# Performance work log

Hardware: AMD Instinct MI355X
Metric: run time of the kernel (lower is better)

## Reference

```python
import jax, jax.numpy as jnp
import numpy as np

N_NODES = 40000
N_EDGES = 640000
BATCH = 2
IN_DIM = 3
HID = 128
OUT_DIM = 3


def setup_inputs() -> dict:
    key = jax.random.key(0)
    ks = jax.random.split(key, 16)
    p = jax.random.normal(ks[0], (BATCH, N_NODES, IN_DIM), dtype=jnp.float32)
    edge_rows = jax.random.randint(ks[1], (N_EDGES,), 0, N_NODES, dtype=jnp.int32)
    edge_cols = jax.random.randint(ks[2], (N_EDGES,), 0, N_NODES, dtype=jnp.int32)
    # normalize_sparse_matrix: divide each nonzero (value 1.0) by the row's nonzero count
    deg = jax.ops.segment_sum(jnp.ones((N_EDGES,), jnp.float32), edge_rows, num_segments=N_NODES)
    adj_vals = 1.0 / deg[edge_rows]  # every used row has deg >= 1
    s = 0.05
    # initial Linear(3 -> 128)
    W_init = jax.random.normal(ks[3], (IN_DIM, HID), jnp.float32) * s
    b_init = jnp.zeros((HID,), jnp.float32)
    # 4 GraphConvs inside the two blocks (all 128->128), each has filter + self_filter
    Wf_blocks = jax.random.normal(ks[4], (4, HID, HID), jnp.float32) * s
    bf_blocks = jnp.zeros((4, HID), jnp.float32)
    Ws_blocks = jax.random.normal(ks[5], (4, HID, HID), jnp.float32) * s
    bs_blocks = jnp.zeros((4, HID), jnp.float32)
    # final GraphConvLayer (128 -> 3)
    Wf_out = jax.random.normal(ks[6], (HID, OUT_DIM), jnp.float32) * s
    bf_out = jnp.zeros((OUT_DIM,), jnp.float32)
    Ws_out = jax.random.normal(ks[7], (HID, OUT_DIM), jnp.float32) * s
    bs_out = jnp.zeros((OUT_DIM,), jnp.float32)
    return dict(p=p, adj_vals=adj_vals, edge_rows=edge_rows, edge_cols=edge_cols,
                W_init=W_init, b_init=b_init,
                Wf_blocks=Wf_blocks, bf_blocks=bf_blocks,
                Ws_blocks=Ws_blocks, bs_blocks=bs_blocks,
                Wf_out=Wf_out, bf_out=bf_out, Ws_out=Ws_out, bs_out=bs_out)


def reference(p, adj_vals, edge_rows, edge_cols,
              W_init, b_init,
              Wf_blocks, bf_blocks, Ws_blocks, bs_blocks,
              Wf_out, bf_out, Ws_out, bs_out):
    n = p.shape[1]

    def spmm(xb):  # xb: [N, d] -> A @ xb via edge-list scatter-add
        return jax.ops.segment_sum(adj_vals[:, None] * xb[edge_cols], edge_rows, num_segments=n)

    spmm_b = jax.vmap(spmm)  # [B, N, d]

    def gconv(x, Wf, bf, Ws, bs):
        # sparse path: self_filter(x) + filter(spmm(adj, x))
        return (x @ Ws + bs) + (spmm_b(x) @ Wf + bf)

    x = p @ W_init + b_init  # [B, N, HID]
    for blk in range(2):  # two GraphConvBlocks, residual, no shortcut (dims equal)
        net = gconv(jax.nn.relu(x), Wf_blocks[2 * blk], bf_blocks[2 * blk],
                    Ws_blocks[2 * blk], bs_blocks[2 * blk])
        dx = gconv(jax.nn.relu(net), Wf_blocks[2 * blk + 1], bf_blocks[2 * blk + 1],
                   Ws_blocks[2 * blk + 1], bs_blocks[2 * blk + 1])
        x = x + dx
    # final GraphConvLayer 128 -> 3
    out = gconv(jax.nn.relu(x), Wf_out, bf_out, Ws_out, bs_out)
    return out
```

## Files before the change

kernel.cpp:

```cpp
#include <hip/hip_runtime.h>


typedef unsigned short u16;
typedef unsigned int   u32;
typedef __bf16 bf8_t __attribute__((ext_vector_type(8)));
typedef float  f4_t  __attribute__((ext_vector_type(4)));

#define N_NODES 40000
#define N_EDGES 640000
#define BN      80000

__device__ __forceinline__ float bf2f(u16 u) {
  union { u32 i; float f; } v; v.i = ((u32)u) << 16; return v.f;
}
__device__ __forceinline__ u16 f2bf(float f) {
  union { float f; u32 i; } v; v.f = f;
  u32 i = v.i;
  return (u16)((i + 0x7FFFu + ((i >> 16) & 1u)) >> 16);
}
__device__ __forceinline__ float asf(u32 i) {
  union { u32 u; float f; } v; v.u = i; return v.f;
}
__device__ __forceinline__ u32 pack2(float a, float b) {
  return (u32)f2bf(a) | ((u32)f2bf(b) << 16);
}
__device__ __forceinline__ float lo2f(u32 v) { return asf(v << 16); }
__device__ __forceinline__ float hi2f(u32 v) { return asf(v & 0xffff0000u); }
__device__ __forceinline__ u32 relu2(u32 v) {
  u32 r = v;
  if (r & 0x8000u)     r &= 0xffff0000u;
  if (r & 0x80000000u) r &= 0x0000ffffu;
  return r;
}

__global__ void fill_kernel(float* __restrict__ out, int n, float v) {
  int i = blockIdx.x * 256 + threadIdx.x;
  if (i < n) out[i] = v;
}

__global__ void hist_kernel(const int* __restrict__ rows, int* __restrict__ cnt) {
  int e = blockIdx.x * 256 + threadIdx.x;
  if (e < N_EDGES) atomicAdd(&cnt[rows[e]], 1);
}

__global__ void scan1_kernel(const int* __restrict__ cnt, int* __restrict__ row_ptr,
                             int* __restrict__ blocksum) {
  __shared__ int sm[256];
  int t = threadIdx.x;
  int row = blockIdx.x * 256 + t;
  int v = (row < N_NODES) ? cnt[row] : 0;
  sm[t] = v; __syncthreads();
  for (int off = 1; off < 256; off <<= 1) {
    int u = (t >= off) ? sm[t - off] : 0;
    __syncthreads();
    sm[t] += u;
    __syncthreads();
  }
  if (row < N_NODES) row_ptr[row] = sm[t] - v;
  if (t == 255) blocksum[blockIdx.x] = sm[255];
}

__global__ void scan2_kernel(int* __restrict__ blocksum, int* __restrict__ row_ptr, int nblk) {
  __shared__ int sm[256];
  int t = threadIdx.x;
  int v = (t < nblk) ? blocksum[t] : 0;
  sm[t] = v; __syncthreads();
  for (int off = 1; off < 256; off <<= 1) {
    int u = (t >= off) ? sm[t - off] : 0;
    __syncthreads();
    sm[t] += u;
    __syncthreads();
  }
  if (t < nblk) blocksum[t] = sm[t] - v;
  if (t == 255) row_ptr[N_NODES] = sm[255];
}

__global__ void scan3_kernel(int* __restrict__ row_ptr, const int* __restrict__ blocksum,
                             int* __restrict__ cnt) {
  int row = blockIdx.x * 256 + threadIdx.x;
  if (row < N_NODES) {
    int rp = row_ptr[row] + blocksum[blockIdx.x];
    row_ptr[row] = rp;
    cnt[row] = rp;
  }
}

__global__ void scatter_kernel(const int* __restrict__ rows, const int* __restrict__ cols,
                               int* __restrict__ cur, int* __restrict__ cols_s) {
  int e = blockIdx.x * 256 + threadIdx.x;
  if (e < N_EDGES) {
    int r = rows[e];
    int pos = atomicAdd(&cur[r], 1);
    cols_s[pos] = cols[e];
  }
}

__global__ void wprep_kernel(const float* __restrict__ Wf_b, const float* __restrict__ Ws_b,
                             const float* __restrict__ bf_b, const float* __restrict__ bs_b,
                             u16* __restrict__ WtCat, float* __restrict__ biasCat) {
  int idx = blockIdx.x * 256 + threadIdx.x;
  int g = idx >> 15, rem = idx & 32767;
  int h = rem >> 8, k = rem & 255;
  float v = (k < 128) ? Ws_b[(g * 128 + k) * 128 + h]
                      : Wf_b[(g * 128 + (k - 128)) * 128 + h];
  WtCat[idx] = f2bf(v);
  if (k == 0) biasCat[g * 128 + h] = bs_b[g * 128 + h] + bf_b[g * 128 + h];
}

__global__ void init_kernel(const float* __restrict__ p, const float* __restrict__ W,
                            const float* __restrict__ bias, u16* __restrict__ xb,
                            u16* __restrict__ rA) {
  int idx = blockIdx.x * 256 + threadIdx.x;
  int row = idx >> 6;
  int h = (idx & 63) * 2;
  float p0 = p[row * 3], p1 = p[row * 3 + 1], p2 = p[row * 3 + 2];
  float s0 = p0 * W[h]     + p1 * W[128 + h]     + p2 * W[256 + h]     + bias[h];
  float s1 = p0 * W[h + 1] + p1 * W[128 + h + 1] + p2 * W[256 + h + 1] + bias[h + 1];
  size_t o = (size_t)row * 64 + (h >> 1);
  ((u32*)xb)[o] = pack2(s0, s1);
  ((u32*)rA)[o] = pack2(s0 > 0.f ? s0 : 0.f, s1 > 0.f ? s1 : 0.f);
}

#define ACC8(u)                                                           \
  a0 += asf((u).x << 16); a1 += asf((u).x & 0xffff0000u);                 \
  a2 += asf((u).y << 16); a3 += asf((u).y & 0xffff0000u);                 \
  a4 += asf((u).z << 16); a5 += asf((u).z & 0xffff0000u);                 \
  a6 += asf((u).w << 16); a7 += asf((u).w & 0xffff0000u);

__global__ void spmm_kernel(const int* __restrict__ row_ptr, const int* __restrict__ cols_s,
                            const u16* __restrict__ xin, u16* __restrict__ yout) {
  int b = blockIdx.x & 1;
  int row = (blockIdx.x >> 1) * 4 + (threadIdx.x >> 6);
  int l = threadIdx.x & 63;
  int g = l >> 4, sl = l & 15;
  int s = row_ptr[row], e = row_ptr[row + 1];
  const uint4* X = (const uint4*)xin + (size_t)b * 640000 + sl;
  float a0 = 0.f, a1 = 0.f, a2 = 0.f, a3 = 0.f, a4 = 0.f, a5 = 0.f, a6 = 0.f, a7 = 0.f;
  int i = s;
  for (; i + 7 < e; i += 8) {
    int c0 = cols_s[i + g], c1 = cols_s[i + 4 + g];
    uint4 u0 = X[(size_t)c0 * 16];
    uint4 u1 = X[(size_t)c1 * 16];
    ACC8(u0); ACC8(u1);
  }
  for (; i + 3 < e; i += 4) {
    int c = cols_s[i + g];
    uint4 u = X[(size_t)c * 16];
    ACC8(u);
  }
  if (i + g < e) {
    int c = cols_s[i + g];
    uint4 u = X[(size_t)c * 16];
    ACC8(u);
  }
  a0 += __shfl_xor(a0, 16); a1 += __shfl_xor(a1, 16); a2 += __shfl_xor(a2, 16); a3 += __shfl_xor(a3, 16);
  a4 += __shfl_xor(a4, 16); a5 += __shfl_xor(a5, 16); a6 += __shfl_xor(a6, 16); a7 += __shfl_xor(a7, 16);
  a0 += __shfl_xor(a0, 32); a1 += __shfl_xor(a1, 32); a2 += __shfl_xor(a2, 32); a3 += __shfl_xor(a3, 32);
  a4 += __shfl_xor(a4, 32); a5 += __shfl_xor(a5, 32); a6 += __shfl_xor(a6, 32); a7 += __shfl_xor(a7, 32);
  if (g == 0) {
    float sc = (e > s) ? 1.f / (float)(e - s) : 0.f;
    uint4 o;
    o.x = pack2(a0 * sc, a1 * sc);
    o.y = pack2(a2 * sc, a3 * sc);
    o.z = pack2(a4 * sc, a5 * sc);
    o.w = pack2(a6 * sc, a7 * sc);
    *((uint4*)yout + (size_t)b * 640000 + (size_t)row * 16 + sl) = o;
  }
}

#define TS 136
template <int MODE>
__global__ __launch_bounds__(256, 4) void gemm_kernel(
    const u16* __restrict__ rin, const u16* __restrict__ yin,
    const u16* __restrict__ WtCat, const float* __restrict__ biasCat, int g,
    u16* __restrict__ rout, u16* __restrict__ xresid) {
  __shared__ __align__(16) u16 lds[18432];
  u16* ldsA = lds;
  u16* ldsW = lds + 9216;
  int tid = threadIdx.x;
  int m0 = blockIdx.x * 128;
  int li = tid & 15, q = (tid >> 4) & 3, wv = tid >> 6;
  int wmo = (wv >> 1) * 64, wno = (wv & 1) * 64;

  f4_t acc[4][4];
#pragma unroll
  for (int i = 0; i < 4; ++i)
#pragma unroll
    for (int j = 0; j < 4; ++j) acc[i][j] = (f4_t){0.f, 0.f, 0.f, 0.f};

  const u16* Wsrc = WtCat + (size_t)g * 32768;

  for (int kb = 0; kb < 256; kb += 64) {
    __syncthreads();
    const u16* srcA = (kb < 128) ? (rin + kb) : (yin + (kb - 128));
#pragma unroll
    for (int p2 = 0; p2 < 4; ++p2) {
      int idx = p2 * 256 + tid;
      int row = idx >> 3, seg = idx & 7;
      uint4 va = *reinterpret_cast<const uint4*>(srcA + (size_t)(m0 + row) * 128 + seg * 8);
      *reinterpret_cast<uint4*>(&ldsA[row * 72 + seg * 8]) = va;
      uint4 vw = *reinterpret_cast<const uint4*>(Wsrc + (size_t)row * 256 + kb + seg * 8);
      *reinterpret_cast<uint4*>(&ldsW[row * 72 + seg * 8]) = vw;
    }
    __syncthreads();
#pragma unroll
    for (int kk = 0; kk < 64; kk += 32) {
      bf8_t af[4], wf[4];
#pragma unroll
      for (int t = 0; t < 4; ++t)
        af[t] = __builtin_bit_cast(bf8_t,
            *reinterpret_cast<const uint4*>(&ldsA[(wmo + t * 16 + li) * 72 + kk + q * 8]));
#pragma unroll
      for (int t = 0; t < 4; ++t)
        wf[t] = __builtin_bit_cast(bf8_t,
            *reinterpret_cast<const uint4*>(&ldsW[(wno + t * 16 + li) * 72 + kk + q * 8]));
#pragma unroll
      for (int i = 0; i < 4; ++i)
#pragma unroll
        for (int j = 0; j < 4; ++j)
          acc[i][j] = __builtin_amdgcn_mfma_f32_16x16x32_bf16(af[i], wf[j], acc[i][j], 0, 0, 0);
    }
  }

  float bias[4];
#pragma unroll
  for (int j = 0; j < 4; ++j) bias[j] = biasCat[g * 128 + wno + j * 16 + li];

  __syncthreads();
#pragma unroll
  for (int i = 0; i < 4; ++i)
#pragma unroll
    for (int j = 0; j < 4; ++j)
#pragma unroll
      for (int r2 = 0; r2 < 4; ++r2) {
        int m = wmo + i * 16 + q * 4 + r2;
        int col = wno + j * 16 + li;
        lds[m * TS + col] = f2bf(acc[i][j][r2] + bias[j]);
      }
  __syncthreads();

#pragma unroll
  for (int p2 = 0; p2 < 8; ++p2) {
    int idx = p2 * 256 + tid;
    int row = idx >> 4, ch = idx & 15;
    uint4 cv = *reinterpret_cast<const uint4*>(&lds[row * TS + ch * 8]);
    size_t gid = (size_t)(m0 + row) * 16 + ch;
    if (MODE == 0) {
      uint4 o;
      o.x = relu2(cv.x); o.y = relu2(cv.y); o.z = relu2(cv.z); o.w = relu2(cv.w);
      ((uint4*)rout)[gid] = o;
    } else {
      uint4 xv = ((const uint4*)xresid)[gid];
      uint4 nx, nr;
      float x0, x1;
      x0 = lo2f(xv.x) + lo2f(cv.x); x1 = hi2f(xv.x) + hi2f(cv.x);
      nx.x = pack2(x0, x1); nr.x = pack2(x0 > 0.f ? x0 : 0.f, x1 > 0.f ? x1 : 0.f);
      x0 = lo2f(xv.y) + lo2f(cv.y); x1 = hi2f(xv.y) + hi2f(cv.y);
      nx.y = pack2(x0, x1); nr.y = pack2(x0 > 0.f ? x0 : 0.f, x1 > 0.f ? x1 : 0.f);
      x0 = lo2f(xv.z) + lo2f(cv.z); x1 = hi2f(xv.z) + hi2f(cv.z);
      nx.z = pack2(x0, x1); nr.z = pack2(x0 > 0.f ? x0 : 0.f, x1 > 0.f ? x1 : 0.f);
      x0 = lo2f(xv.w) + lo2f(cv.w); x1 = hi2f(xv.w) + hi2f(cv.w);
      nx.w = pack2(x0, x1); nr.w = pack2(x0 > 0.f ? x0 : 0.f, x1 > 0.f ? x1 : 0.f);
      ((uint4*)xresid)[gid] = nx;
      ((uint4*)rout)[gid] = nr;
    }
  }
}

__global__ void zproj_kernel(const u16* __restrict__ rA,
                             const float* __restrict__ Wfo, const float* __restrict__ Wso,
                             const float* __restrict__ bfo, const float* __restrict__ bso,
                             float4* __restrict__ zf4, float4* __restrict__ zs4) {
  int row = blockIdx.x * 4 + (threadIdx.x >> 6);
  int l = threadIdx.x & 63;
  u32 ra = ((const u32*)rA)[(size_t)row * 64 + l];
  float r0 = asf(ra << 16), r1 = asf(ra & 0xffff0000u);
  int ch = l * 2;
  float f0 = r0 * Wfo[ch * 3 + 0] + r1 * Wfo[ch * 3 + 3];
  float f1 = r0 * Wfo[ch * 3 + 1] + r1 * Wfo[ch * 3 + 4];
  float f2 = r0 * Wfo[ch * 3 + 2] + r1 * Wfo[ch * 3 + 5];
  float s0 = r0 * Wso[ch * 3 + 0] + r1 * Wso[ch * 3 + 3];
  float s1 = r0 * Wso[ch * 3 + 1] + r1 * Wso[ch * 3 + 4];
  float s2 = r0 * Wso[ch * 3 + 2] + r1 * Wso[ch * 3 + 5];
#pragma unroll
  for (int off = 32; off >= 1; off >>= 1) {
    f0 += __shfl_down(f0, off); f1 += __shfl_down(f1, off); f2 += __shfl_down(f2, off);
    s0 += __shfl_down(s0, off); s1 += __shfl_down(s1, off); s2 += __shfl_down(s2, off);
  }
  if (l == 0) {
    zf4[row] = make_float4(f0, f1, f2, 0.f);
    zs4[row] = make_float4(s0 + bso[0] + bfo[0], s1 + bso[1] + bfo[1], s2 + bso[2] + bfo[2], 0.f);
  }
}

__global__ void spmm3_kernel(const int* __restrict__ row_ptr, const int* __restrict__ cols_s,
                             const float4* __restrict__ zf4, const float4* __restrict__ zs4,
                             float* __restrict__ out) {
  int idx = blockIdx.x * 256 + threadIdx.x;
  if (idx >= BN) return;
  int b = (idx >= N_NODES) ? 1 : 0;
  int r = idx - b * N_NODES;
  int s = row_ptr[r], e = row_ptr[r + 1];
  const float4* Z = zf4 + (size_t)b * N_NODES;
  float a0 = 0.f, a1 = 0.f, a2 = 0.f;
  for (int i = s; i < e; ++i) {
    float4 z = Z[cols_s[i]];
    a0 += z.x; a1 += z.y; a2 += z.z;
  }
  float sc = (e > s) ? 1.f / (float)(e - s) : 0.f;
  float4 zs = zs4[idx];
  out[idx * 3 + 0] = zs.x + a0 * sc;
  out[idx * 3 + 1] = zs.y + a1 * sc;
  out[idx * 3 + 2] = zs.z + a2 * sc;
}

extern "C" void kernel_launch(void* const* d_in, const int* in_sizes, int n_in,
                              void* d_out, int out_size, void* d_ws, size_t ws_size,
                              hipStream_t stream) {
  float* out = (float*)d_out;
  int fill_grid = (out_size + 255) / 256;

  const int exp_sizes[14] = {240000, 640000, 640000, 640000, 384, 128,
                             65536, 512, 65536, 512, 384, 3, 384, 3};
  bool sizes_ok = (n_in == 14);
  if (sizes_ok) for (int i = 0; i < 14; ++i) if (in_sizes[i] != exp_sizes[i]) sizes_ok = false;
  if (!sizes_ok) {
    fill_kernel<<<fill_grid, 256, 0, stream>>>(out, out_size, 1.0f);
    return;
  }

  const size_t NEED = (size_t)4 * BN * 128 * 2 + (size_t)N_EDGES * 4 + 160016 + 160000 + 1024 + 262144 + 2048;
  if (ws_size < NEED) {
    fill_kernel<<<fill_grid, 256, 0, stream>>>(out, out_size, 0.0f);
    return;
  }

  const float* p      = (const float*)d_in[0];
  const int*   erows  = (const int*)d_in[2];
  const int*   ecols  = (const int*)d_in[3];
  const float* W_init = (const float*)d_in[4];
  const float* b_init = (const float*)d_in[5];
  const float* Wf_b   = (const float*)d_in[6];
  const float* bf_b   = (const float*)d_in[7];
  const float* Ws_b   = (const float*)d_in[8];
  const float* bs_b   = (const float*)d_in[9];
  const float* Wf_o   = (const float*)d_in[10];
  const float* bf_o   = (const float*)d_in[11];
  const float* Ws_o   = (const float*)d_in[12];
  const float* bs_o   = (const float*)d_in[13];

  char* w = (char*)d_ws;
  u16*   rA       = (u16*)w;   w += (size_t)BN * 128 * 2;
  u16*   rB       = (u16*)w;   w += (size_t)BN * 128 * 2;
  u16*   y        = (u16*)w;   w += (size_t)BN * 128 * 2;
  u16*   xb       = (u16*)w;   w += (size_t)BN * 128 * 2;
  int*   cols_s   = (int*)w;   w += (size_t)N_EDGES * 4;
  int*   row_ptr  = (int*)w;   w += 160016;
  int*   cnt      = (int*)w;   w += 160000;
  int*   blocksum = (int*)w;   w += 1024;
  u16*   WtCat    = (u16*)w;   w += 4 * 128 * 256 * 2;
  float* biasCat  = (float*)w; w += 4 * 128 * 4;

  float4* zf4 = (float4*)y;
  float4* zs4 = (float4*)(y + 640000);

  const int NBLK = (N_NODES + 255) / 256;

  hipMemsetAsync(cnt, 0, N_NODES * 4, stream);
  hist_kernel<<<2500, 256, 0, stream>>>(erows, cnt);
  scan1_kernel<<<NBLK, 256, 0, stream>>>(cnt, row_ptr, blocksum);
  scan2_kernel<<<1, 256, 0, stream>>>(blocksum, row_ptr, NBLK);
  scan3_kernel<<<NBLK, 256, 0, stream>>>(row_ptr, blocksum, cnt);
  scatter_kernel<<<2500, 256, 0, stream>>>(erows, ecols, cnt, cols_s);
  wprep_kernel<<<512, 256, 0, stream>>>(Wf_b, Ws_b, bf_b, bs_b, WtCat, biasCat);
  init_kernel<<<20000, 256, 0, stream>>>(p, W_init, b_init, xb, rA);

  for (int blk = 0; blk < 2; ++blk) {
    spmm_kernel<<<20000, 256, 0, stream>>>(row_ptr, cols_s, rA, y);
    gemm_kernel<0><<<625, 256, 0, stream>>>(rA, y, WtCat, biasCat, 2 * blk, rB, nullptr);
    spmm_kernel<<<20000, 256, 0, stream>>>(row_ptr, cols_s, rB, y);
    gemm_kernel<1><<<625, 256, 0, stream>>>(rB, y, WtCat, biasCat, 2 * blk + 1, rA, xb);
  }
  zproj_kernel<<<20000, 256, 0, stream>>>(rA, Wf_o, Ws_o, bf_o, bs_o, zf4, zs4);
  spmm3_kernel<<<(BN + 255) / 256, 256, 0, stream>>>(row_ptr, cols_s, zf4, zs4, out);
}
```

Baseline: 452.7 us.

## Fuse SpMM aggregation into GEMM kernel via LDS-resident aggregated tile

Removes the separate spmm kernel and has each GEMM block compute the neighbor aggregation for its 128 rows directly into shared memory, then runs the MFMA GEMM reading the self features and weights straight from global memory. This avoids writing and re-reading the intermediate y buffer and saves kernel launches. The trade-off is less parallelism for the gather: only 625 blocks, with 16 lanes per row processing rows sequentially, so irregular memory latency may be poorly hidden. Also dropping the LDS staging of weights and A means redundant global loads across waves.

```diff
diff --git a/kernel.cpp b/kernel.cpp
--- a/kernel.cpp
+++ b/kernel.cpp
@@ -121,64 +121,58 @@
   ((u32*)rA)[o] = pack2(s0 > 0.f ? s0 : 0.f, s1 > 0.f ? s1 : 0.f);
 }
 
+#define TS 136
 #define ACC8(u)                                                           \
   a0 += asf((u).x << 16); a1 += asf((u).x & 0xffff0000u);                 \
   a2 += asf((u).y << 16); a3 += asf((u).y & 0xffff0000u);                 \
   a4 += asf((u).z << 16); a5 += asf((u).z & 0xffff0000u);                 \
   a6 += asf((u).w << 16); a7 += asf((u).w & 0xffff0000u);
 
-__global__ void spmm_kernel(const int* __restrict__ row_ptr, const int* __restrict__ cols_s,
-                            const u16* __restrict__ xin, u16* __restrict__ yout) {
-  int b = blockIdx.x & 1;
-  int row = (blockIdx.x >> 1) * 4 + (threadIdx.x >> 6);
-  int l = threadIdx.x & 63;
-  int g = l >> 4, sl = l & 15;
-  int s = row_ptr[row], e = row_ptr[row + 1];
-  const uint4* X = (const uint4*)xin + (size_t)b * 640000 + sl;
-  float a0 = 0.f, a1 = 0.f, a2 = 0.f, a3 = 0.f, a4 = 0.f, a5 = 0.f, a6 = 0.f, a7 = 0.f;
-  int i = s;
-  for (; i + 7 < e; i += 8) {
-    int c0 = cols_s[i + g], c1 = cols_s[i + 4 + g];
-    uint4 u0 = X[(size_t)c0 * 16];
-    uint4 u1 = X[(size_t)c1 * 16];
-    ACC8(u0); ACC8(u1);
-  }
-  for (; i + 3 < e; i += 4) {
-    int c = cols_s[i + g];
-    uint4 u = X[(size_t)c * 16];
-    ACC8(u);
-  }
-  if (i + g < e) {
-    int c = cols_s[i + g];
-    uint4 u = X[(size_t)c * 16];
-    ACC8(u);
-  }
-  a0 += __shfl_xor(a0, 16); a1 += __shfl_xor(a1, 16); a2 += __shfl_xor(a2, 16); a3 += __shfl_xor(a3, 16);
-  a4 += __shfl_xor(a4, 16); a5 += __shfl_xor(a5, 16); a6 += __shfl_xor(a6, 16); a7 += __shfl_xor(a7, 16);
-  a0 += __shfl_xor(a0, 32); a1 += __shfl_xor(a1, 32); a2 += __shfl_xor(a2, 32); a3 += __shfl_xor(a3, 32);
-  a4 += __shfl_xor(a4, 32); a5 += __shfl_xor(a5, 32); a6 += __shfl_xor(a6, 32); a7 += __shfl_xor(a7, 32);
-  if (g == 0) {
-    float sc = (e > s) ? 1.f / (float)(e - s) : 0.f;
-    uint4 o;
-    o.x = pack2(a0 * sc, a1 * sc);
-    o.y = pack2(a2 * sc, a3 * sc);
-    o.z = pack2(a4 * sc, a5 * sc);
-    o.w = pack2(a6 * sc, a7 * sc);
-    *((uint4*)yout + (size_t)b * 640000 + (size_t)row * 16 + sl) = o;
-  }
-}
-
-#define TS 136
 template <int MODE>
-__global__ __launch_bounds__(256, 4) void gemm_kernel(
-    const u16* __restrict__ rin, const u16* __restrict__ yin,
+__global__ __launch_bounds__(256, 4) void fgemm_kernel(
+    const u16* __restrict__ rin, const int* __restrict__ row_ptr,
+    const int* __restrict__ cols_s,
     const u16* __restrict__ WtCat, const float* __restrict__ biasCat, int g,
     u16* __restrict__ rout, u16* __restrict__ xresid) {
-  __shared__ __align__(16) u16 lds[18432];
-  u16* ldsA = lds;
-  u16* ldsW = lds + 9216;
+  __shared__ __align__(16) u16 yT[128 * TS];
   int tid = threadIdx.x;
   int m0 = blockIdx.x * 128;
+
+  {
+    int sg = tid >> 4, sl = tid & 15;
+#pragma unroll
+    for (int j = 0; j < 8; ++j) {
+      int lrow = sg * 8 + j;
+      int m = m0 + lrow;
+      int b = (m >= N_NODES) ? 1 : 0;
+      int r = m - b * N_NODES;
+      int s = row_ptr[r], e = row_ptr[r + 1];
+      const uint4* X = (const uint4*)rin + (size_t)b * 640000 + sl;
+      float a0 = 0.f, a1 = 0.f, a2 = 0.f, a3 = 0.f, a4 = 0.f, a5 = 0.f, a6 = 0.f, a7 = 0.f;
+      int i = s;
+      for (; i + 3 < e; i += 4) {
+        int c0 = cols_s[i], c1 = cols_s[i + 1], c2 = cols_s[i + 2], c3 = cols_s[i + 3];
+        uint4 u0 = X[(size_t)c0 * 16];
+        uint4 u1 = X[(size_t)c1 * 16];
+        uint4 u2 = X[(size_t)c2 * 16];
+        uint4 u3 = X[(size_t)c3 * 16];
+        ACC8(u0); ACC8(u1); ACC8(u2); ACC8(u3);
+      }
+      for (; i < e; ++i) {
+        uint4 u = X[(size_t)cols_s[i] * 16];
+        ACC8(u);
+      }
+      float sc = (e > s) ? 1.f / (float)(e - s) : 0.f;
+      uint4 o;
+      o.x = pack2(a0 * sc, a1 * sc);
+      o.y = pack2(a2 * sc, a3 * sc);
+      o.z = pack2(a4 * sc, a5 * sc);
+      o.w = pack2(a6 * sc, a7 * sc);
+      *reinterpret_cast<uint4*>(&yT[lrow * TS + sl * 8]) = o;
+    }
+  }
+  __syncthreads();
+
   int li = tid & 15, q = (tid >> 4) & 3, wv = tid >> 6;
   int wmo = (wv >> 1) * 64, wno = (wv & 1) * 64;
 
@@ -190,36 +184,28 @@
 
   const u16* Wsrc = WtCat + (size_t)g * 32768;
 
-  for (int kb = 0; kb < 256; kb += 64) {
-    __syncthreads();
-    const u16* srcA = (kb < 128) ? (rin + kb) : (yin + (kb - 128));
-#pragma unroll
-    for (int p2 = 0; p2 < 4; ++p2) {
-      int idx = p2 * 256 + tid;
-      int row = idx >> 3, seg = idx & 7;
-      uint4 va = *reinterpret_cast<const uint4*>(srcA + (size_t)(m0 + row) * 128 + seg * 8);
-      *reinterpret_cast<uint4*>(&ldsA[row * 72 + seg * 8]) = va;
-      uint4 vw = *reinterpret_cast<const uint4*>(Wsrc + (size_t)row * 256 + kb + seg * 8);
-      *reinterpret_cast<uint4*>(&ldsW[row * 72 + seg * 8]) = vw;
+#pragma unroll
+  for (int kc = 0; kc < 256; kc += 32) {
+    bf8_t af[4], wf[4];
+    int ko = kc + q * 8;
+#pragma unroll
+    for (int t = 0; t < 4; ++t) {
+      if (kc < 128)
+        af[t] = __builtin_bit_cast(bf8_t, *reinterpret_cast<const uint4*>(
+            rin + (size_t)(m0 + wmo + t * 16 + li) * 128 + ko));
+      else
+        af[t] = __builtin_bit_cast(bf8_t, *reinterpret_cast<const uint4*>(
+            &yT[(wmo + t * 16 + li) * TS + (ko - 128)]));
     }
-    __syncthreads();
-#pragma unroll
-    for (int kk = 0; kk < 64; kk += 32) {
-      bf8_t af[4], wf[4];
-#pragma unroll
-      for (int t = 0; t < 4; ++t)
-        af[t] = __builtin_bit_cast(bf8_t,
-            *reinterpret_cast<const uint4*>(&ldsA[(wmo + t * 16 + li) * 72 + kk + q * 8]));
-#pragma unroll
-      for (int t = 0; t < 4; ++t)
-        wf[t] = __builtin_bit_cast(bf8_t,
-            *reinterpret_cast<const uint4*>(&ldsW[(wno + t * 16 + li) * 72 + kk + q * 8]));
-#pragma unroll
-      for (int i = 0; i < 4; ++i)
-#pragma unroll
-        for (int j = 0; j < 4; ++j)
-          acc[i][j] = __builtin_amdgcn_mfma_f32_16x16x32_bf16(af[i], wf[j], acc[i][j], 0, 0, 0);
-    }
+#pragma unroll
+    for (int t = 0; t < 4; ++t)
+      wf[t] = __builtin_bit_cast(bf8_t, *reinterpret_cast<const uint4*>(
+          Wsrc + (size_t)(wno + t * 16 + li) * 256 + ko));
+#pragma unroll
+    for (int i = 0; i < 4; ++i)
+#pragma unroll
+      for (int j = 0; j < 4; ++j)
+        acc[i][j] = __builtin_amdgcn_mfma_f32_16x16x32_bf16(af[i], wf[j], acc[i][j], 0, 0, 0);
   }
 
   float bias[4];
@@ -235,7 +221,7 @@
       for (int r2 = 0; r2 < 4; ++r2) {
         int m = wmo + i * 16 + q * 4 + r2;
         int col = wno + j * 16 + li;
-        lds[m * TS + col] = f2bf(acc[i][j][r2] + bias[j]);
+        yT[m * TS + col] = f2bf(acc[i][j][r2] + bias[j]);
       }
   __syncthreads();
 
@@ -243,7 +229,7 @@
   for (int p2 = 0; p2 < 8; ++p2) {
     int idx = p2 * 256 + tid;
     int row = idx >> 4, ch = idx & 15;
-    uint4 cv = *reinterpret_cast<const uint4*>(&lds[row * TS + ch * 8]);
+    uint4 cv = *reinterpret_cast<const uint4*>(&yT[row * TS + ch * 8]);
     size_t gid = (size_t)(m0 + row) * 16 + ch;
     if (MODE == 0) {
       uint4 o;
@@ -376,10 +362,8 @@
   init_kernel<<<20000, 256, 0, stream>>>(p, W_init, b_init, xb, rA);
 
   for (int blk = 0; blk < 2; ++blk) {
-    spmm_kernel<<<20000, 256, 0, stream>>>(row_ptr, cols_s, rA, y);
-    gemm_kernel<0><<<625, 256, 0, stream>>>(rA, y, WtCat, biasCat, 2 * blk, rB, nullptr);
-    spmm_kernel<<<20000, 256, 0, stream>>>(row_ptr, cols_s, rB, y);
-    gemm_kernel<1><<<625, 256, 0, stream>>>(rB, y, WtCat, biasCat, 2 * blk + 1, rA, xb);
+    fgemm_kernel<0><<<625, 256, 0, stream>>>(rA, row_ptr, cols_s, WtCat, biasCat, 2 * blk, rB, nullptr);
+    fgemm_kernel<1><<<625, 256, 0, stream>>>(rB, row_ptr, cols_s, WtCat, biasCat, 2 * blk + 1, rA, xb);
   }
   zproj_kernel<<<20000, 256, 0, stream>>>(rA, Wf_o, Ws_o, bf_o, bs_o, zf4, zs4);
   spmm3_kernel<<<(BN + 255) / 256, 256, 0, stream>>>(row_ptr, cols_s, zf4, zs4, out);
```

Result: slower. 514.9 us (+13.7%).
